# Kernel tuning notes

Measured on AMD Instinct MI355X. Metric: run time of the kernel, lower is better.

Reference implementation:

```python
import jax, jax.numpy as jnp
import numpy as np
import math

B, N, D_MODEL, H = 4, 2048, 1024, 16
D_HEAD = D_MODEL // H

def setup_inputs() -> dict:
    key = jax.random.key(0)
    ks = jax.random.split(key, 9)
    s = 1.0 / math.sqrt(D_MODEL)
    inp = {
        "X_Q": jax.random.normal(ks[0], (B, N, D_MODEL), jnp.float32),
        "X_K": jax.random.normal(ks[1], (B, N, D_MODEL), jnp.float32),
        "X_V": jax.random.normal(ks[2], (B, N, D_MODEL), jnp.float32),
        # stacked per-head projection weights: [H, D_MODEL, D_HEAD] (y = x @ W + b)
        "Wq": jax.random.uniform(ks[3], (H, D_MODEL, D_HEAD), jnp.float32, -s, s),
        "Wk": jax.random.uniform(ks[4], (H, D_MODEL, D_HEAD), jnp.float32, -s, s),
        "Wv": jax.random.uniform(ks[5], (H, D_MODEL, D_HEAD), jnp.float32, -s, s),
        "bq": jax.random.uniform(ks[6], (H, D_HEAD), jnp.float32, -s, s),
        "bk": jax.random.uniform(ks[7], (H, D_HEAD), jnp.float32, -s, s),
        "bv": jax.random.uniform(ks[8], (H, D_HEAD), jnp.float32, -s, s),
    }
    return inp

def reference(X_Q, X_K, X_V, Wq, Wk, Wv, bq, bk, bv):
    # per-head projections, batched over heads: [B, H, N, D_HEAD]
    Q = jnp.einsum("bnd,hde->bhne", X_Q, Wq) + bq[None, :, None, :]
    K = jnp.einsum("bnd,hde->bhne", X_K, Wk) + bk[None, :, None, :]
    V = jnp.einsum("bnd,hde->bhne", X_V, Wv) + bv[None, :, None, :]
    scores = jnp.einsum("bhne,bhme->bhnm", Q, K)  # [B, H, N, N]
    # causal (att_mask=True): mask strictly-upper-triangular with -inf
    causal = jnp.tril(jnp.ones((N, N), dtype=bool))
    scores = jnp.where(causal[None, None], scores, -jnp.inf)
    # original divides AFTER masking; -inf stays -inf so equivalent
    probs = jax.nn.softmax(scores / math.sqrt(D_HEAD), axis=-1)
    out = jnp.einsum("bhnm,bhme->bhne", probs, V)  # [B, H, N, D_HEAD]
    # concat heads along feature dim
    return out.transpose(0, 2, 1, 3).reshape(B, N, D_MODEL)
```

## Files before the change

### kernel.cpp

```cpp
#include <hip/hip_runtime.h>

typedef _Float16 half8  __attribute__((ext_vector_type(8)));
typedef _Float16 half4v __attribute__((ext_vector_type(4)));
typedef _Float16 half2v __attribute__((ext_vector_type(2)));
typedef float    floatx4 __attribute__((ext_vector_type(4)));

#define B_   4
#define N_   2048
#define DM_  1024
#define H_   16
#define DH_  64

static const size_t XEL = (size_t)B_ * N_ * DM_;
static const size_t WEL = (size_t)DM_ * DM_;
static const size_t QEL = (size_t)B_ * H_ * N_ * DH_;

#define GLOAD_LDS16(src, dst) \
  __builtin_amdgcn_global_load_lds((const __attribute__((address_space(1))) void*)(src), \
                                   (__attribute__((address_space(3))) void*)(dst), 16, 0, 0)

__global__ void cvt_x(const float* __restrict__ x0, const float* __restrict__ x1,
                      const float* __restrict__ x2, _Float16* __restrict__ out) {
  const int z = blockIdx.z;
  const float* x = (z == 0) ? x0 : (z == 1 ? x1 : x2);
  _Float16* o = out + (size_t)z * XEL;
  const size_t i = ((size_t)blockIdx.x * 256 + threadIdx.x) * 4;
  float4 v = *(const float4*)(x + i);
  half4v h;
  h[0] = (_Float16)v.x; h[1] = (_Float16)v.y; h[2] = (_Float16)v.z; h[3] = (_Float16)v.w;
  *(half4v*)(o + i) = h;
}

__global__ void cvt_w(const float* __restrict__ w0, const float* __restrict__ w1,
                      const float* __restrict__ w2, _Float16* __restrict__ out) {
  const int z = blockIdx.z;
  const float* w = (z == 0) ? w0 : (z == 1 ? w1 : w2);
  _Float16* o = out + (size_t)z * WEL;
  const int idx = blockIdx.x * 256 + threadIdx.x;
  const int n = idx >> 10, k = idx & 1023;
  const int h = n >> 6, e = n & 63;
  o[idx] = (_Float16)w[((size_t)h * 1024 + k) * 64 + e];
}

__global__ __launch_bounds__(256, 3) void qkv_gemm(const _Float16* __restrict__ X16,
                                                   const _Float16* __restrict__ W16t,
                                                   const float* __restrict__ b0,
                                                   const float* __restrict__ b1,
                                                   const float* __restrict__ b2,
                                                   _Float16* __restrict__ QKV) {
  __shared__ char smem[49152];
  const int lid = blockIdx.x;
  const int win = lid >> 6;
  const int i6  = lid & 63;
  const int n0i = i6 >> 3;
  const int c   = i6 & 7;
  const int g   = win * 8 + c;
  const int z   = g >> 6;
  const int row0 = (g & 63) * 128;
  const int n0   = n0i * 128;

  const _Float16* X = X16 + (size_t)z * XEL;
  const _Float16* W = W16t + (size_t)z * WEL;
  const float* bias = (z == 0) ? b0 : (z == 1 ? b1 : b2);
  const float osc = (z == 0) ? 0.18033688011112042f : 1.0f;
  _Float16* out = QKV + (size_t)z * QEL;

  const int tid = threadIdx.x;
  const int w   = tid >> 6;
  const int l   = tid & 63;
  const int lg  = l >> 4, lr = l & 15;
  const int wm  = w >> 1, wn = w & 1;

  floatx4 zf = {0.f, 0.f, 0.f, 0.f};
  floatx4 acc[4][4];
#pragma unroll
  for (int mi = 0; mi < 4; ++mi)
#pragma unroll
    for (int ni = 0; ni < 4; ++ni) acc[mi][ni] = zf;

  auto STAGE = [&](int kt, int bufc) {
    char* Ab = smem + bufc * 16384;
    char* Bb = Ab + 8192;
    const int k0 = kt * 32;
#pragma unroll
    for (int i = 0; i < 2; ++i) {
      const int q   = i * 4 + w;
      const int row = q * 16 + (l >> 2);
      const int kb  = (l & 3) ^ ((row >> 1) & 3);
      GLOAD_LDS16(X + (size_t)(row0 + row) * 1024 + k0 + kb * 8, Ab + q * 1024);
      GLOAD_LDS16(W + (size_t)(n0  + row) * 1024 + k0 + kb * 8, Bb + q * 1024);
    }
  };

  const int chq = (lg ^ ((lr >> 1) & 3)) * 16;
  const int aA  = wm * 4096 + lr * 64 + chq;
  const int aB  = wn * 4096 + lr * 64 + chq;

  STAGE(0, 0);
  STAGE(1, 1);
  int rb = 0, wb = 2;

  for (int kt = 0; kt < 32; ++kt) {
    if (kt + 2 < 32) {
      STAGE(kt + 2, wb);
      wb = (wb == 2) ? 0 : wb + 1;
      asm volatile("s_waitcnt vmcnt(8)" ::: "memory");
    } else if (kt == 30) {
      asm volatile("s_waitcnt vmcnt(4)" ::: "memory");
    } else {
      asm volatile("s_waitcnt vmcnt(0)" ::: "memory");
    }
    __builtin_amdgcn_s_barrier();
    __builtin_amdgcn_sched_barrier(0);

    const char* Al = smem + rb * 16384;
    const char* Bl = Al + 8192;
    half8 af[4], bf[4];
#pragma unroll
    for (int mi = 0; mi < 4; ++mi) af[mi] = *(const half8*)(Al + aA + mi * 1024);
#pragma unroll
    for (int ni = 0; ni < 4; ++ni) bf[ni] = *(const half8*)(Bl + aB + ni * 1024);
#pragma unroll
    for (int mi = 0; mi < 4; ++mi)
#pragma unroll
      for (int ni = 0; ni < 4; ++ni)
        acc[mi][ni] = __builtin_amdgcn_mfma_f32_16x16x32_f16(af[mi], bf[ni], acc[mi][ni], 0, 0, 0);

    __builtin_amdgcn_sched_barrier(0);
    __builtin_amdgcn_s_barrier();
    rb = (rb == 2) ? 0 : rb + 1;
  }

#pragma unroll
  for (int mi = 0; mi < 4; ++mi)
#pragma unroll
    for (int ni = 0; ni < 4; ++ni) {
      const int gc = n0 + wn * 64 + ni * 16 + lr;
      const float bv = bias[gc];
      const int h = gc >> 6, e = gc & 63;
#pragma unroll
      for (int j = 0; j < 4; ++j) {
        const int gr = row0 + wm * 64 + mi * 16 + lg * 4 + j;
        const int b = gr >> 11, n = gr & 2047;
        out[(((size_t)(b * 16 + h)) * 2048 + n) * 64 + e] = (_Float16)((acc[mi][ni][j] + bv) * osc);
      }
    }
}

__global__ void vtrans(const _Float16* __restrict__ V16, _Float16* __restrict__ Vt) {
  __shared__ _Float16 t[64 * 72];
  const int bh = blockIdx.y;
  const int n0 = blockIdx.x * 64;
  const int tid = threadIdx.x;
#pragma unroll
  for (int it = 0; it < 2; ++it) {
    const int L = it * 256 + tid;
    const int n = L >> 3, cb = L & 7;
    half8 v = *(const half8*)(V16 + ((size_t)bh * 2048 + n0 + n) * 64 + cb * 8);
    *(half8*)(t + n * 72 + cb * 8) = v;
  }
  __syncthreads();
#pragma unroll
  for (int it = 0; it < 2; ++it) {
    const int L = it * 256 + tid;
    const int d = L >> 3, cb = L & 7;
    half8 v;
#pragma unroll
    for (int u = 0; u < 8; ++u) v[u] = t[(cb * 8 + u) * 72 + d];
    *(half8*)(Vt + ((size_t)bh * 64 + d) * 2048 + n0 + cb * 8) = v;
  }
}

__global__ __launch_bounds__(512, 4) void attn(const _Float16* __restrict__ Q16,
                                               const _Float16* __restrict__ K16,
                                               const _Float16* __restrict__ Vt16,
                                               float* __restrict__ out) {
  __shared__ char smem[49152];
  const int lid = blockIdx.x;
  const int bh = (lid & 7) | ((lid >> 6) << 3);
  const int bx = (lid >> 3) & 7;
  const int tid = threadIdx.x;
  const int w = tid >> 6, l = tid & 63;
  const int lg = l >> 4, lr = l & 15;
  const int b = bh >> 4, h = bh & 15;

  const int sz = lr & 7;
  const int aK0 = lr * 128 + ((lg ^ sz) * 16);
  const int aK1 = lr * 128 + (((4 + lg) ^ sz) * 16);
  const int pbase = 32768 + w * 2048 + lr * 128;
  int aPw[4];
#pragma unroll
  for (int cb = 0; cb < 4; ++cb)
    aPw[cb] = pbase + (((2 * cb + (lg >> 1)) ^ sz) << 4) + ((lg & 1) * 8);
  const int aPr0 = pbase + ((lg ^ sz) << 4);
  const int aPr1 = pbase + (((4 + lg) ^ sz) << 4);

  int cur = 0;

  auto STAGE = [&](int t, int bufc) {
    const int c0t = t * 64;
    char* Kb = smem + bufc * 16384;
    char* Vb = Kb + 8192;
    const int row = w * 8 + (l >> 3);
    const int kb = l & 7;
    const int ks = (kb ^ (row & 7)) << 3;
    GLOAD_LDS16(K16 + ((size_t)bh * 2048 + c0t + row) * 64 + ks, Kb + w * 1024);
    GLOAD_LDS16(Vt16 + ((size_t)bh * 64 + row) * 2048 + c0t + ks, Vb + w * 1024);
  };

  for (int ph = 0; ph < 2; ++ph) {
    const int qt = ph ? (15 - bx) : bx;
    const int q0 = qt * 128;
    const int wr0 = q0 + w * 16;
    const int nt = 2 * (qt + 1);

    half8 qf[2];
#pragma unroll
    for (int kk = 0; kk < 2; ++kk)
      qf[kk] = *(const half8*)(Q16 + ((size_t)bh * 2048 + wr0 + lr) * 64 + kk * 32 + lg * 8);

    floatx4 zf = {0.f, 0.f, 0.f, 0.f};
    floatx4 O[4];
#pragma unroll
    for (int dt = 0; dt < 4; ++dt) O[dt] = zf;
    float mrow = -3.0e38f;
    float lden = 0.f;

    STAGE(0, cur);

    for (int t = 0; t < nt; ++t) {
      if (t + 1 < nt) {
        STAGE(t + 1, cur ^ 1);
        asm volatile("s_waitcnt vmcnt(2)" ::: "memory");
      } else {
        asm volatile("s_waitcnt vmcnt(0)" ::: "memory");
      }
      __builtin_amdgcn_s_barrier();
      __builtin_amdgcn_sched_barrier(0);

      const int c0 = t * 64;
      const char* Kb = smem + cur * 16384;

      if (c0 <= wr0 + 15) {
        floatx4 s[4];
#pragma unroll
        for (int cb = 0; cb < 4; ++cb) s[cb] = zf;
#pragma unroll
        for (int cb = 0; cb < 4; ++cb) {
          half8 kf = *(const half8*)(Kb + aK0 + cb * 2048);
          s[cb] = __builtin_amdgcn_mfma_f32_16x16x32_f16(kf, qf[0], s[cb], 0, 0, 0);
        }
#pragma unroll
        for (int cb = 0; cb < 4; ++cb) {
          half8 kf = *(const half8*)(Kb + aK1 + cb * 2048);
          s[cb] = __builtin_amdgcn_mfma_f32_16x16x32_f16(kf, qf[1], s[cb], 0, 0, 0);
        }

        float tm = -3.0e38f;
        if (c0 + 63 > wr0) {
          const int r = wr0 + lr;
#pragma unroll
          for (int cb = 0; cb < 4; ++cb)
#pragma unroll
            for (int j = 0; j < 4; ++j) {
              const int cc = c0 + cb * 16 + lg * 4 + j;
              float x = s[cb][j];
              x = (cc > r) ? -3.0e38f : x;
              s[cb][j] = x;
              tm = fmaxf(tm, x);
            }
        } else {
#pragma unroll
          for (int cb = 0; cb < 4; ++cb) {
            const float m01 = fmaxf(s[cb][0], s[cb][1]);
            const float m23 = fmaxf(s[cb][2], s[cb][3]);
            tm = fmaxf(tm, fmaxf(m01, m23));
          }
        }
        tm = fmaxf(tm, __shfl_xor(tm, 16, 64));
        tm = fmaxf(tm, __shfl_xor(tm, 32, 64));

        float scl = 1.0f;
        if (__any(tm > mrow + 8.0f)) {
          const float mn = fmaxf(mrow, tm);
          scl = __builtin_amdgcn_exp2f(mrow - mn);
          mrow = mn;
          const float s0 = __shfl(scl, lg * 4 + 0, 64);
          const float s1 = __shfl(scl, lg * 4 + 1, 64);
          const float s2 = __shfl(scl, lg * 4 + 2, 64);
          const float s3 = __shfl(scl, lg * 4 + 3, 64);
#pragma unroll
          for (int dt = 0; dt < 4; ++dt) {
            O[dt][0] *= s0; O[dt][1] *= s1; O[dt][2] *= s2; O[dt][3] *= s3;
          }
        }

        float tsum = 0.f;
#pragma unroll
        for (int cb = 0; cb < 4; ++cb)
#pragma unroll
          for (int j = 0; j < 4; ++j) {
            const float p = __builtin_amdgcn_exp2f(s[cb][j] - mrow);
            s[cb][j] = p;
            tsum += p;
          }
        tsum += __shfl_xor(tsum, 16, 64);
        tsum += __shfl_xor(tsum, 32, 64);
        lden = lden * scl + tsum;

#pragma unroll
        for (int cb = 0; cb < 4; ++cb) {
          half4v hv;
          hv[0] = (_Float16)s[cb][0]; hv[1] = (_Float16)s[cb][1];
          hv[2] = (_Float16)s[cb][2]; hv[3] = (_Float16)s[cb][3];
          *(half4v*)(smem + aPw[cb]) = hv;
        }
        asm volatile("s_waitcnt lgkmcnt(0)" ::: "memory");
        __builtin_amdgcn_sched_barrier(0);

        {
          half8 pa = *(const half8*)(smem + aPr0);
#pragma unroll
          for (int dt = 0; dt < 4; ++dt) {
            half8 vb = *(const half8*)(Kb + 8192 + aK0 + dt * 2048);
            O[dt] = __builtin_amdgcn_mfma_f32_16x16x32_f16(pa, vb, O[dt], 0, 0, 0);
          }
          pa = *(const half8*)(smem + aPr1);
#pragma unroll
          for (int dt = 0; dt < 4; ++dt) {
            half8 vb = *(const half8*)(Kb + 8192 + aK1 + dt * 2048);
            O[dt] = __builtin_amdgcn_mfma_f32_16x16x32_f16(pa, vb, O[dt], 0, 0, 0);
          }
        }
      }

      __builtin_amdgcn_sched_barrier(0);
      __builtin_amdgcn_s_barrier();
      cur ^= 1;
    }

    float inv[4];
#pragma unroll
    for (int j = 0; j < 4; ++j) {
      const float lj = __shfl(lden, lg * 4 + j, 64);
      inv[j] = 1.0f / lj;
    }
#pragma unroll
    for (int dt = 0; dt < 4; ++dt)
#pragma unroll
      for (int j = 0; j < 4; ++j) {
        const int n = wr0 + lg * 4 + j;
        out[((size_t)(b * 2048 + n)) * 1024 + h * 64 + dt * 16 + lr] = O[dt][j] * inv[j];
      }
  }
}

extern "C" void kernel_launch(void* const* d_in, const int* in_sizes, int n_in,
                              void* d_out, int out_size, void* d_ws, size_t ws_size,
                              hipStream_t stream) {
  const float* XQ = (const float*)d_in[0];
  const float* XK = (const float*)d_in[1];
  const float* XV = (const float*)d_in[2];
  const float* Wq = (const float*)d_in[3];
  const float* Wk = (const float*)d_in[4];
  const float* Wv = (const float*)d_in[5];
  const float* bq = (const float*)d_in[6];
  const float* bk = (const float*)d_in[7];
  const float* bv = (const float*)d_in[8];

  char* ws = (char*)d_ws;
  _Float16* X16  = (_Float16*)(ws + 0);
  _Float16* W16t = (_Float16*)(ws + 50331648);
  _Float16* QKV  = (_Float16*)(ws + 56623104);
  _Float16* Vt   = (_Float16*)(ws + 106954752);

  cvt_x<<<dim3(8192, 1, 3), 256, 0, stream>>>(XQ, XK, XV, X16);
  cvt_w<<<dim3(4096, 1, 3), 256, 0, stream>>>(Wq, Wk, Wv, W16t);
  qkv_gemm<<<dim3(1536), 256, 0, stream>>>(X16, W16t, bq, bk, bv, QKV);
  vtrans<<<dim3(32, 64), 256, 0, stream>>>(QKV + 2 * QEL, Vt);
  attn<<<dim3(512), 512, 0, stream>>>(QKV, QKV + QEL, Vt, (float*)d_out);
}
```

Baseline: 173.6 us.

## Fuse fp32-to-fp16 activation conversion into QKV GEMM register-staged loads

Removes the separate cvt_x kernel. The QKV GEMM now loads fp32 activations straight into registers, converts them to fp16 and writes them into swizzled LDS, while weights still use direct global-to-LDS loads. This avoids writing and re-reading a 48 MB fp16 copy of X. In exchange the pipeline drops from triple buffering with fine-grained vmcnt waits to double buffering with __syncthreads, global reads of X double in bytes, and occupancy rises to 4 blocks because LDS use is smaller.

```diff
diff --git a/kernel.cpp b/kernel.cpp
--- a/kernel.cpp
+++ b/kernel.cpp
@@ -18,18 +18,6 @@
 #define GLOAD_LDS16(src, dst) \
   __builtin_amdgcn_global_load_lds((const __attribute__((address_space(1))) void*)(src), \
                                    (__attribute__((address_space(3))) void*)(dst), 16, 0, 0)
-
-__global__ void cvt_x(const float* __restrict__ x0, const float* __restrict__ x1,
-                      const float* __restrict__ x2, _Float16* __restrict__ out) {
-  const int z = blockIdx.z;
-  const float* x = (z == 0) ? x0 : (z == 1 ? x1 : x2);
-  _Float16* o = out + (size_t)z * XEL;
-  const size_t i = ((size_t)blockIdx.x * 256 + threadIdx.x) * 4;
-  float4 v = *(const float4*)(x + i);
-  half4v h;
-  h[0] = (_Float16)v.x; h[1] = (_Float16)v.y; h[2] = (_Float16)v.z; h[3] = (_Float16)v.w;
-  *(half4v*)(o + i) = h;
-}
 
 __global__ void cvt_w(const float* __restrict__ w0, const float* __restrict__ w1,
                       const float* __restrict__ w2, _Float16* __restrict__ out) {
@@ -42,13 +30,15 @@
   o[idx] = (_Float16)w[((size_t)h * 1024 + k) * 64 + e];
 }
 
-__global__ __launch_bounds__(256, 3) void qkv_gemm(const _Float16* __restrict__ X16,
+__global__ __launch_bounds__(256, 4) void qkv_gemm(const float* __restrict__ XQ32,
+                                                   const float* __restrict__ XK32,
+                                                   const float* __restrict__ XV32,
                                                    const _Float16* __restrict__ W16t,
                                                    const float* __restrict__ b0,
                                                    const float* __restrict__ b1,
                                                    const float* __restrict__ b2,
                                                    _Float16* __restrict__ QKV) {
-  __shared__ char smem[49152];
+  __shared__ char smem[32768];
   const int lid = blockIdx.x;
   const int win = lid >> 6;
   const int i6  = lid & 63;
@@ -59,7 +49,7 @@
   const int row0 = (g & 63) * 128;
   const int n0   = n0i * 128;
 
-  const _Float16* X = X16 + (size_t)z * XEL;
+  const float* X32 = (z == 0) ? XQ32 : (z == 1 ? XK32 : XV32);
   const _Float16* W = W16t + (size_t)z * WEL;
   const float* bias = (z == 0) ? b0 : (z == 1 ? b1 : b2);
   const float osc = (z == 0) ? 0.18033688011112042f : 1.0f;
@@ -78,57 +68,74 @@
 #pragma unroll
     for (int ni = 0; ni < 4; ++ni) acc[mi][ni] = zf;
 
-  auto STAGE = [&](int kt, int bufc) {
+  floatx4 xr[2][2];
+  auto XLOAD = [&](int kt) {
+    const int k0 = kt * 32;
+#pragma unroll
+    for (int i = 0; i < 2; ++i) {
+      const int C = i * 256 + tid, row = C >> 2, cj = C & 3;
+      const int kc = cj ^ ((row >> 1) & 3);
+      const float* p = X32 + (size_t)(row0 + row) * 1024 + k0 + kc * 8;
+      xr[i][0] = *(const floatx4*)p;
+      xr[i][1] = *(const floatx4*)(p + 4);
+    }
+  };
+  auto XWRITE = [&](int bufc) {
     char* Ab = smem + bufc * 16384;
-    char* Bb = Ab + 8192;
+#pragma unroll
+    for (int i = 0; i < 2; ++i) {
+      const int C = i * 256 + tid, row = C >> 2, cj = C & 3;
+      half8 hv;
+#pragma unroll
+      for (int u = 0; u < 4; ++u) {
+        hv[u]     = (_Float16)xr[i][0][u];
+        hv[4 + u] = (_Float16)xr[i][1][u];
+      }
+      *(half8*)(Ab + row * 64 + cj * 16) = hv;
+    }
+  };
+  auto WSTAGE = [&](int kt, int bufc) {
+    char* Bb = smem + bufc * 16384 + 8192;
     const int k0 = kt * 32;
 #pragma unroll
     for (int i = 0; i < 2; ++i) {
       const int q   = i * 4 + w;
       const int row = q * 16 + (l >> 2);
       const int kb  = (l & 3) ^ ((row >> 1) & 3);
-      GLOAD_LDS16(X + (size_t)(row0 + row) * 1024 + k0 + kb * 8, Ab + q * 1024);
-      GLOAD_LDS16(W + (size_t)(n0  + row) * 1024 + k0 + kb * 8, Bb + q * 1024);
+      GLOAD_LDS16(W + (size_t)(n0 + row) * 1024 + k0 + kb * 8, Bb + q * 1024);
     }
   };
 
   const int chq = (lg ^ ((lr >> 1) & 3)) * 16;
   const int aA  = wm * 4096 + lr * 64 + chq;
-  const int aB  = wn * 4096 + lr * 64 + chq;
-
-  STAGE(0, 0);
-  STAGE(1, 1);
-  int rb = 0, wb = 2;
+  const int aB  = 8192 + wn * 4096 + lr * 64 + chq;
+
+  XLOAD(0);
+  WSTAGE(0, 0);
+  XWRITE(0);
+  __syncthreads();
 
   for (int kt = 0; kt < 32; ++kt) {
-    if (kt + 2 < 32) {
-      STAGE(kt + 2, wb);
-      wb = (wb == 2) ? 0 : wb + 1;
-      asm volatile("s_waitcnt vmcnt(8)" ::: "memory");
-    } else if (kt == 30) {
-      asm volatile("s_waitcnt vmcnt(4)" ::: "memory");
-    } else {
-      asm volatile("s_waitcnt vmcnt(0)" ::: "memory");
-    }
-    __builtin_amdgcn_s_barrier();
-    __builtin_amdgcn_sched_barrier(0);
-
-    const char* Al = smem + rb * 16384;
-    const char* Bl = Al + 8192;
+    const int cur = kt & 1, nxt = cur ^ 1;
+    if (kt + 1 < 32) {
+      XLOAD(kt + 1);
+      WSTAGE(kt + 1, nxt);
+    }
+
+    const char* Al = smem + cur * 16384;
     half8 af[4], bf[4];
 #pragma unroll
     for (int mi = 0; mi < 4; ++mi) af[mi] = *(const half8*)(Al + aA + mi * 1024);
 #pragma unroll
-    for (int ni = 0; ni < 4; ++ni) bf[ni] = *(const half8*)(Bl + aB + ni * 1024);
+    for (int ni = 0; ni < 4; ++ni) bf[ni] = *(const half8*)(Al + aB + ni * 1024);
 #pragma unroll
     for (int mi = 0; mi < 4; ++mi)
 #pragma unroll
       for (int ni = 0; ni < 4; ++ni)
         acc[mi][ni] = __builtin_amdgcn_mfma_f32_16x16x32_f16(af[mi], bf[ni], acc[mi][ni], 0, 0, 0);
 
-    __builtin_amdgcn_sched_barrier(0);
-    __builtin_amdgcn_s_barrier();
-    rb = (rb == 2) ? 0 : rb + 1;
+    if (kt + 1 < 32) XWRITE(nxt);
+    __syncthreads();
   }
 
 #pragma unroll
@@ -369,14 +376,12 @@
   const float* bv = (const float*)d_in[8];
 
   char* ws = (char*)d_ws;
-  _Float16* X16  = (_Float16*)(ws + 0);
-  _Float16* W16t = (_Float16*)(ws + 50331648);
-  _Float16* QKV  = (_Float16*)(ws + 56623104);
-  _Float16* Vt   = (_Float16*)(ws + 106954752);
-
-  cvt_x<<<dim3(8192, 1, 3), 256, 0, stream>>>(XQ, XK, XV, X16);
+  _Float16* W16t = (_Float16*)(ws + 0);
+  _Float16* QKV  = (_Float16*)(ws + 6291456);
+  _Float16* Vt   = (_Float16*)(ws + 56623104);
+
   cvt_w<<<dim3(4096, 1, 3), 256, 0, stream>>>(Wq, Wk, Wv, W16t);
-  qkv_gemm<<<dim3(1536), 256, 0, stream>>>(X16, W16t, bq, bk, bv, QKV);
+  qkv_gemm<<<dim3(1536), 256, 0, stream>>>(XQ, XK, XV, W16t, bq, bk, bv, QKV);
   vtrans<<<dim3(32, 64), 256, 0, stream>>>(QKV + 2 * QEL, Vt);
   attn<<<dim3(512), 512, 0, stream>>>(QKV, QKV + QEL, Vt, (float*)d_out);
 }
```

Result: faster. 158.5 us (-8.7%).
